# Kernel optimization log

Hardware: AMD Instinct MI355X
Metric: run time of the kernel (lower is better)

The kernel has to match this reference:

```python
import jax, jax.numpy as jnp
import numpy as np

B = 1024        # batch_size (len(c_ids))
D = 128         # dim_proto
N_AFE_A = 2     # len(AFE_a_ids_selected) == l_a
N_AFE_R = 2     # len(AFE_r_ids_selected) == l_r
S = 16          # sum(n_nbs_per_hop) = 10 + 6
A = 4096        # num_atoms (active codebook rows)
L = N_AFE_A + N_AFE_R * S  # 34


def _normalize(x, eps=1e-12):
    # torch F.normalize(dim=-1): x / max(||x||_2, eps)
    n = jnp.linalg.norm(x, axis=-1, keepdims=True)
    return x / jnp.maximum(n, eps)


def setup_inputs() -> dict:
    key = jax.random.key(0)
    k1, k2, k3 = jax.random.split(key, 3)
    embeddings = jax.random.normal(k1, (B, L, D), dtype=jnp.float32)
    atoms = jax.random.uniform(k2, (A, D), dtype=jnp.float32, minval=0.0, maxval=0.5)
    W_att = jax.random.normal(k3, ((N_AFE_A + N_AFE_R * S) * D, N_AFE_R * S + N_AFE_A), dtype=jnp.float32) * 0.02
    b_att = jnp.zeros((N_AFE_R * S + N_AFE_A,), dtype=jnp.float32)
    return {"embeddings": embeddings, "atoms": atoms, "W_att": W_att, "b_att": b_att}


def reference(embeddings, atoms, W_att, b_att):
    atoms_n = _normalize(atoms)  # F.normalize(self.atoms[0:num_atoms], dim=-1), [A, D]

    # --- attribute emb sets: embeddings[:, i, :] for i in range(n_AFE_a) ---
    attr = embeddings[:, :N_AFE_A, :]                                 # [B, la, D]
    soft_a = jnp.einsum('bld,ad->bla', attr, atoms_n)                 # similarity vs codebook
    hard_a = (soft_a == soft_a.max(axis=-1, keepdims=True)).astype(jnp.float32)
    assoc_a = jnp.einsum('bla,ad->bld', hard_a, atoms)                # one-hot @ atoms (lookup)

    # --- relational emb sets: chunks of size S, flattened to [B*S, D] in torch ---
    rel = embeddings[:, N_AFE_A:, :].reshape(B, N_AFE_R, S, D)
    soft_r = jnp.einsum('brsd,ad->brsa', rel, atoms_n)
    hard_r = (soft_r == soft_r.max(axis=-1, keepdims=True)).astype(jnp.float32)
    assoc_r = jnp.einsum('brsa,ad->brsd', hard_r, atoms).reshape(B, N_AFE_R * S, D)

    # per-row L2 normalize each associated prototype, then concat along slot dim
    assoc = jnp.concatenate([_normalize(assoc_a), _normalize(assoc_r)], axis=1)  # [B, la+lr*S, D]

    # attention aggregation: Linear over flattened slots, then bmm
    a = assoc.reshape(B, (N_AFE_A + N_AFE_R * S) * D)
    att = a @ W_att + b_att                                           # [B, la+lr*S]
    obj_embs = _normalize(jnp.einsum('bl,bld->bd', att, assoc))       # [B, D]
    return obj_embs
```

## Files before the change

kernel.cpp:

```cpp
#include <hip/hip_runtime.h>
#include <math.h>

#define BB 1024
#define LL 34
#define DD 128
#define AA 4096
#define NROWS (BB * LL)
#define RTILES (NROWS / 16)
#define ATILES (AA / 16)
#define NSPLIT 8
#define TPS (ATILES / NSPLIT)
#define NCHUNK (TPS / 4)
#define TAU 2.5e-3f
#define SCOREBLKS ((RTILES / 16) * NSPLIT)
#define GTABBLKS (LL * 32)

typedef _Float16 f16;
typedef _Float16 f16x8 __attribute__((ext_vector_type(8)));
typedef float f32x4  __attribute__((ext_vector_type(4)));

#define OFF_EMBA   0u
#define OFF_ATOMB  8912896u
#define OFF_WFRAG  9961472u
#define OFF_G      10379264u
#define OFF_PQ     30433280u
#define OFF_INVN64 34889728u
#define OFF_INVNF  34922496u

__global__ __launch_bounds__(256) void k_prep(const float* __restrict__ emb,
                                              const float* __restrict__ atoms,
                                              const float* __restrict__ W,
                                              double* __restrict__ invn64,
                                              float* __restrict__ invnF,
                                              f16x8* __restrict__ embA,
                                              f16x8* __restrict__ atomB,
                                              f16x8* __restrict__ wfrag) {
    __shared__ __align__(16) float stbuf[4608];
    __shared__ double part[16][17];
    const int bid = blockIdx.x;
    const int tid = threadIdx.x;

    if (bid < RTILES + ATILES) {
        const bool isAtom = (bid >= RTILES);
        const int tile = isAtom ? bid - RTILES : bid;
        const float* src = (isAtom ? atoms : emb) + (size_t)tile * 2048;
        float4* st4 = (float4*)stbuf;
        for (int i = tid; i < 512; i += 256) {
            int row = i >> 5, c4 = i & 31;
            st4[row * 33 + c4] = ((const float4*)src)[i];
        }
        __syncthreads();

        const int ks = tid >> 6, l = tid & 63;
        const int m = l & 15, koff4 = ((l >> 4) << 1) + (ks << 3);
        float4 f0 = st4[m * 33 + koff4];
        float4 f1 = st4[m * 33 + koff4 + 1];
        float xs[8] = {f0.x, f0.y, f0.z, f0.w, f1.x, f1.y, f1.z, f1.w};

        if (!isAtom) {
            f16x8 h;
            #pragma unroll
            for (int j = 0; j < 8; j++) h[j] = (f16)xs[j];
            embA[(size_t)(tile * 4 + ks) * 64 + l] = h;
        } else {
            double ssq = 0.0;
            #pragma unroll
            for (int j = 0; j < 8; j++) ssq += (double)xs[j] * xs[j];
            part[m][ks * 4 + (l >> 4)] = ssq;
            __syncthreads();
            double tot = 0.0;
            #pragma unroll
            for (int q = 0; q < 16; q++) tot += part[m][q];
            double n = sqrt(tot);
            if (n < 1e-12) n = 1e-12;
            double inv = 1.0 / n;
            float invf = (float)inv;
            f16x8 h;
            #pragma unroll
            for (int j = 0; j < 8; j++) h[j] = (f16)(xs[j] * invf);
            if (ks == 0 && (l >> 4) == 0) {
                invn64[tile * 16 + m] = inv;
                invnF[tile * 16 + m] = invf;
            }
            atomB[(size_t)(tile * 4 + ks) * 64 + l] = h;
        }
    } else {
        const int l = bid - RTILES - ATILES;
        const float* wsrc = W + (size_t)l * 128 * LL;
        for (int i = tid; i < 128 * LL; i += 256) {
            int row = i / LL, j = i - row * LL;
            stbuf[row * 35 + j] = wsrc[i];
        }
        __syncthreads();
        for (int s = tid; s < 768; s += 256) {
            int lane = s & 63, ksnt = s >> 6;
            int ks = ksnt & 3, nt = ksnt >> 2;
            int j = nt * 16 + (lane & 15);
            int kb = ks * 32 + ((lane >> 4) << 3);
            f16x8 h;
            if (j < LL) {
                #pragma unroll
                for (int jj = 0; jj < 8; jj++) h[jj] = (f16)stbuf[(kb + jj) * 35 + j];
            } else {
                #pragma unroll
                for (int jj = 0; jj < 8; jj++) h[jj] = (f16)0.f;
            }
            wfrag[(size_t)((l * 3 + nt) * 4 + ks) * 64 + lane] = h;
        }
    }
}

__global__ __launch_bounds__(256, 3) void k_score(const f16x8* __restrict__ embA,
                                                  const char* __restrict__ atomB,
                                                  const f16x8* __restrict__ wfrag,
                                                  float* __restrict__ G,
                                                  float4* __restrict__ pq) {
    __shared__ __align__(16) char shmem[32768];
    const int tid = threadIdx.x;
    const int w = tid >> 6, l = tid & 63;

    if (blockIdx.x >= SCOREBLKS) {
        const int gb = blockIdx.x - SCOREBLKS;
        const int ll = gb >> 5, ab = gb & 31;
        float* gs = (float*)shmem;

        f16x8 bw[3][4];
        #pragma unroll
        for (int nt = 0; nt < 3; nt++)
            #pragma unroll
            for (int ks = 0; ks < 4; ks++)
                bw[nt][ks] = wfrag[(size_t)((ll * 3 + nt) * 4 + ks) * 64 + l];

        const int col = l & 15, rq = (l >> 4) * 4;
        #pragma unroll
        for (int t = 0; t < 2; t++) {
            int atile = ab * 8 + w * 2 + t;
            f16x8 ah[4];
            #pragma unroll
            for (int ks = 0; ks < 4; ks++)
                ah[ks] = *(const f16x8*)(atomB + ((size_t)(atile * 4 + ks) * 64 + l) * 16);
            f32x4 acc[3];
            #pragma unroll
            for (int nt = 0; nt < 3; nt++) acc[nt] = (f32x4){0.f, 0.f, 0.f, 0.f};
            #pragma unroll
            for (int ks = 0; ks < 4; ks++)
                #pragma unroll
                for (int nt = 0; nt < 3; nt++)
                    acc[nt] = __builtin_amdgcn_mfma_f32_16x16x32_f16(ah[ks], bw[nt][ks], acc[nt], 0, 0, 0);
            int aloc0 = (w * 2 + t) * 16 + rq;
            #pragma unroll
            for (int nt = 0; nt < 3; nt++) {
                int j = nt * 16 + col;
                if (j < LL) {
                    #pragma unroll
                    for (int r = 0; r < 4; r++)
                        gs[(aloc0 + r) * 36 + j] = acc[nt][r];
                }
            }
        }
        __syncthreads();
        float* Gl = G + ((size_t)ll * 4096 + ab * 128) * 36;
        for (int i = tid; i < 128 * 36; i += 256) Gl[i] = gs[i];
        return;
    }

    char (*sbuf)[16384] = (char(*)[16384])shmem;
    const int sp = blockIdx.x / 136, rb = blockIdx.x - sp * 136;
    const int rt0 = rb * 16 + w * 4;

    f16x8 a[4][4];
    #pragma unroll
    for (int f = 0; f < 4; f++)
        #pragma unroll
        for (int ks = 0; ks < 4; ks++)
            a[f][ks] = embA[(size_t)((rt0 + f) * 4 + ks) * 64 + l];

    float v1[16], v2[16];
    #pragma unroll
    for (int s = 0; s < 16; s++) { v1[s] = -3e38f; v2[s] = -3e38f; }

    #define STAGE(C, BUF)                                                          \
        {                                                                          \
            size_t _tb = (size_t)(sp * TPS + (C) * 4) * 4096;                      \
            _Pragma("unroll")                                                      \
            for (int r = 0; r < 4; r++) {                                          \
                const char* _src = atomB + _tb + r * 4096;                         \
                uint32_t* _dst = (uint32_t*)(&sbuf[BUF][0] + r * 4096 + w * 1024); \
                __builtin_amdgcn_global_load_lds((const uint32_t*)(_src + tid * 16), \
                                                 _dst, 16, 0, 0);                  \
            }                                                                      \
        }

    STAGE(0, 0);
    __syncthreads();

    for (int c = 0; c < NCHUNK; c++) {
        const int buf = c & 1;
        if (c + 1 < NCHUNK) STAGE(c + 1, buf ^ 1);

        #pragma unroll
        for (int tt = 0; tt < 4; tt++) {
            f16x8 bh[4];
            #pragma unroll
            for (int ks = 0; ks < 4; ks++)
                bh[ks] = *(const f16x8*)(&sbuf[buf][0] + tt * 4096 + ks * 1024 + l * 16);
            f32x4 acc[4];
            #pragma unroll
            for (int f = 0; f < 4; f++) acc[f] = (f32x4){0.f, 0.f, 0.f, 0.f};
            #pragma unroll
            for (int ks = 0; ks < 4; ks++)
                #pragma unroll
                for (int f = 0; f < 4; f++)
                    acc[f] = __builtin_amdgcn_mfma_f32_16x16x32_f16(a[f][ks], bh[ks], acc[f], 0, 0, 0);
            const unsigned tl = (unsigned)(c * 4 + tt);
            #pragma unroll
            for (int f = 0; f < 4; f++)
                #pragma unroll
                for (int r = 0; r < 4; r++) {
                    int s = f * 4 + r;
                    float xq = __uint_as_float((__float_as_uint(acc[f][r]) & 0xFFFFFFE0u) | tl);
                    v2[s] = __builtin_amdgcn_fmed3f(xq, v1[s], v2[s]);
                    v1[s] = fmaxf(v1[s], xq);
                }
        }
        __syncthreads();
    }
    #undef STAGE

    float vv1[16], vv2[16];
    int jj1[16], jj2[16];
    const int col = l & 15;
    #pragma unroll
    for (int s = 0; s < 16; s++) {
        unsigned u1 = __float_as_uint(v1[s]);
        unsigned u2 = __float_as_uint(v2[s]);
        vv1[s] = __uint_as_float(u1 & 0xFFFFFFE0u);
        vv2[s] = __uint_as_float(u2 & 0xFFFFFFE0u);
        jj1[s] = (sp * TPS + (int)(u1 & 31u)) * 16 + col;
        jj2[s] = (sp * TPS + (int)(u2 & 31u)) * 16 + col;
    }

    #pragma unroll
    for (int m = 1; m <= 8; m <<= 1) {
        #pragma unroll
        for (int s = 0; s < 16; s++) {
            float ov1 = __shfl_xor(vv1[s], m);
            float ov2 = __shfl_xor(vv2[s], m);
            int   oi1 = __shfl_xor(jj1[s], m);
            int   oi2 = __shfl_xor(jj2[s], m);
            bool sel = ov1 > vv1[s];
            float lv  = sel ? vv1[s] : ov1;
            int   li  = sel ? jj1[s] : oi1;
            float wv2 = sel ? ov2 : vv2[s];
            int   wi2 = sel ? oi2 : jj2[s];
            vv1[s] = sel ? ov1 : vv1[s];
            jj1[s] = sel ? oi1 : jj1[s];
            bool s2 = lv > wv2;
            vv2[s] = s2 ? lv : wv2;
            jj2[s] = s2 ? li : wi2;
        }
    }

    if ((l & 15) == 0) {
        int q = l >> 4;
        #pragma unroll
        for (int f = 0; f < 4; f++)
            #pragma unroll
            for (int r = 0; r < 4; r++) {
                int s = f * 4 + r;
                int row = (rt0 + f) * 16 + q * 4 + r;
                float4 o;
                o.x = vv1[s];
                o.y = vv2[s];
                o.z = __int_as_float(jj1[s]);
                o.w = __int_as_float(jj2[s]);
                pq[(size_t)row * NSPLIT + sp] = o;
            }
    }
}

__global__ __launch_bounds__(256) void k_epilogue(const float4* __restrict__ pq,
                                                  const float* __restrict__ emb,
                                                  const float* __restrict__ atoms,
                                                  const double* __restrict__ invn64,
                                                  const float* __restrict__ invnF,
                                                  const float* __restrict__ G,
                                                  const float* __restrict__ b_att,
                                                  float* __restrict__ out) {
    __shared__ __align__(16) float assoc[LL * DD];
    __shared__ __align__(16) float4 pqS[LL][NSPLIT];
    __shared__ int   amaxS[LL];
    __shared__ float invS[LL];
    __shared__ float attS[LL];
    __shared__ float wsum[4][40];
    __shared__ float sqw[4];
    __shared__ int   flagCnt;
    __shared__ int   flagRow[LL];

    const int b = blockIdx.x, tid = threadIdx.x;
    const int wid = tid >> 6, lane = tid & 63;

    if (tid == 0) flagCnt = 0;
    for (int i = tid; i < LL * NSPLIT; i += 256)
        pqS[i >> 3][i & 7] = pq[(size_t)(b * LL + (i >> 3)) * NSPLIT + (i & 7)];
    __syncthreads();

    if (tid < LL) {
        float V1 = -3e38f, V2 = -3e38f;
        int I1 = 0;
        #pragma unroll
        for (int sp = 0; sp < NSPLIT; sp++) {
            float4 qv = pqS[tid][sp];
            float a1 = qv.x, a2 = qv.y;
            int   j1 = __float_as_int(qv.z);
            bool sel = a1 > V1;
            float lv  = sel ? V1 : a1;
            float wv2 = sel ? a2 : V2;
            V1 = sel ? a1 : V1;
            I1 = sel ? j1 : I1;
            V2 = fmaxf(lv, wv2);
        }
        amaxS[tid] = I1;
        if (V1 - V2 < TAU) {
            int k = atomicAdd(&flagCnt, 1);
            flagRow[k] = tid;
        }
    }
    __syncthreads();

    const int cnt = flagCnt;
    for (int fi = wid; fi < cnt; fi += 4) {
        int row = flagRow[fi];
        const float2 ev = ((const float2*)(emb + (size_t)(b * LL + row) * DD))[lane];
        double bestS = -1e300;
        int bestI = 0x7fffffff;
        for (int sp = 0; sp < NSPLIT; sp++) {
            float4 qv = pqS[row][sp];
            #pragma unroll
            for (int h = 0; h < 2; h++) {
                int idx = __float_as_int(h ? qv.w : qv.z);
                const float2 av = ((const float2*)(atoms + (size_t)idx * DD))[lane];
                double p = (double)ev.x * av.x + (double)ev.y * av.y;
                #pragma unroll
                for (int m = 1; m <= 32; m <<= 1) p += __shfl_xor(p, m);
                double sc = p * invn64[idx];
                if (sc > bestS || (sc == bestS && idx < bestI)) { bestS = sc; bestI = idx; }
            }
        }
        if (lane == 0) amaxS[row] = bestI;
    }
    __syncthreads();

    if (tid < LL) invS[tid] = invnF[amaxS[tid]];
    if (lane < LL) {
        float ga = 0.f;
        for (int ll = wid; ll < LL; ll += 4)
            ga += G[((size_t)ll * 4096 + amaxS[ll]) * 36 + lane];
        wsum[wid][lane] = ga;
    }
    __syncthreads();

    for (int idx = tid; idx < LL * DD; idx += 256) {
        int ll = idx >> 7, d = idx & 127;
        assoc[idx] = atoms[(size_t)amaxS[ll] * DD + d] * invS[ll];
    }
    if (tid < LL)
        attS[tid] = b_att[tid] + wsum[0][tid] + wsum[1][tid] + wsum[2][tid] + wsum[3][tid];
    __syncthreads();

    float o = 0.0f;
    if (tid < DD) {
        #pragma unroll
        for (int ll = 0; ll < LL; ll++) o = fmaf(attS[ll], assoc[ll * DD + tid], o);
    }
    float sq = (tid < DD) ? o * o : 0.0f;
    #pragma unroll
    for (int off = 32; off; off >>= 1) sq += __shfl_xor(sq, off);
    if (lane == 0) sqw[wid] = sq;
    __syncthreads();
    float tot = sqw[0] + sqw[1] + sqw[2] + sqw[3];
    float n = sqrtf(tot);
    float inv = 1.0f / fmaxf(n, 1e-12f);
    if (tid < DD) out[(size_t)b * DD + tid] = o * inv;
}

extern "C" void kernel_launch(void* const* d_in, const int* in_sizes, int n_in,
                              void* d_out, int out_size, void* d_ws, size_t ws_size,
                              hipStream_t stream) {
    const float* emb   = (const float*)d_in[0];
    const float* atoms = (const float*)d_in[1];
    const float* W     = (const float*)d_in[2];
    const float* b_att = (const float*)d_in[3];
    float* out = (float*)d_out;

    char* ws = (char*)d_ws;
    f16x8*  embA   = (f16x8*)(ws + OFF_EMBA);
    char*   atomB  = (char*)(ws + OFF_ATOMB);
    f16x8*  wfrag  = (f16x8*)(ws + OFF_WFRAG);
    float*  G      = (float*)(ws + OFF_G);
    float4* pq     = (float4*)(ws + OFF_PQ);
    double* invn64 = (double*)(ws + OFF_INVN64);
    float*  invnF  = (float*)(ws + OFF_INVNF);

    k_prep<<<RTILES + ATILES + LL, 256, 0, stream>>>(emb, atoms, W, invn64, invnF,
                                                     embA, (f16x8*)atomB, wfrag);
    k_score<<<SCOREBLKS + GTABBLKS, 256, 0, stream>>>(embA, atomB, wfrag, G, pq);
    k_epilogue<<<BB, 256, 0, stream>>>(pq, emb, atoms, invn64, invnF, G, b_att, out);
}
```

Before: 157.6 us.

## Load atom tiles directly into registers instead of staging through LDS

The score loop stops staging atom tiles into double-buffered shared memory with global_load_lds and per-chunk barriers. Each wave now loads its B fragments straight from global memory into registers, using a two-register software pipeline across tiles. This removes the LDS traffic and the __syncthreads calls. In exchange every wave fetches the same atom data on its own, which leans on L1/L2, and it uses more registers.

```diff
diff --git a/kernel.cpp b/kernel.cpp
--- a/kernel.cpp
+++ b/kernel.cpp
@@ -10,7 +10,6 @@
 #define ATILES (AA / 16)
 #define NSPLIT 8
 #define TPS (ATILES / NSPLIT)
-#define NCHUNK (TPS / 4)
 #define TAU 2.5e-3f
 #define SCOREBLKS ((RTILES / 16) * NSPLIT)
 #define GTABBLKS (LL * 32)
@@ -115,14 +114,13 @@
                                                   const f16x8* __restrict__ wfrag,
                                                   float* __restrict__ G,
                                                   float4* __restrict__ pq) {
-    __shared__ __align__(16) char shmem[32768];
     const int tid = threadIdx.x;
     const int w = tid >> 6, l = tid & 63;
 
     if (blockIdx.x >= SCOREBLKS) {
+        __shared__ __align__(16) float gs[128 * 36];
         const int gb = blockIdx.x - SCOREBLKS;
         const int ll = gb >> 5, ab = gb & 31;
-        float* gs = (float*)shmem;
 
         f16x8 bw[3][4];
         #pragma unroll
@@ -164,7 +162,6 @@
         return;
     }
 
-    char (*sbuf)[16384] = (char(*)[16384])shmem;
     const int sp = blockIdx.x / 136, rb = blockIdx.x - sp * 136;
     const int rt0 = rb * 16 + w * 4;
 
@@ -179,53 +176,47 @@
     #pragma unroll
     for (int s = 0; s < 16; s++) { v1[s] = -3e38f; v2[s] = -3e38f; }
 
-    #define STAGE(C, BUF)                                                          \
-        {                                                                          \
-            size_t _tb = (size_t)(sp * TPS + (C) * 4) * 4096;                      \
-            _Pragma("unroll")                                                      \
-            for (int r = 0; r < 4; r++) {                                          \
-                const char* _src = atomB + _tb + r * 4096;                         \
-                uint32_t* _dst = (uint32_t*)(&sbuf[BUF][0] + r * 4096 + w * 1024); \
-                __builtin_amdgcn_global_load_lds((const uint32_t*)(_src + tid * 16), \
-                                                 _dst, 16, 0, 0);                  \
-            }                                                                      \
-        }
-
-    STAGE(0, 0);
-    __syncthreads();
-
-    for (int c = 0; c < NCHUNK; c++) {
-        const int buf = c & 1;
-        if (c + 1 < NCHUNK) STAGE(c + 1, buf ^ 1);
-
-        #pragma unroll
-        for (int tt = 0; tt < 4; tt++) {
-            f16x8 bh[4];
-            #pragma unroll
-            for (int ks = 0; ks < 4; ks++)
-                bh[ks] = *(const f16x8*)(&sbuf[buf][0] + tt * 4096 + ks * 1024 + l * 16);
-            f32x4 acc[4];
-            #pragma unroll
-            for (int f = 0; f < 4; f++) acc[f] = (f32x4){0.f, 0.f, 0.f, 0.f};
-            #pragma unroll
-            for (int ks = 0; ks < 4; ks++)
-                #pragma unroll
-                for (int f = 0; f < 4; f++)
-                    acc[f] = __builtin_amdgcn_mfma_f32_16x16x32_f16(a[f][ks], bh[ks], acc[f], 0, 0, 0);
-            const unsigned tl = (unsigned)(c * 4 + tt);
-            #pragma unroll
-            for (int f = 0; f < 4; f++)
-                #pragma unroll
-                for (int r = 0; r < 4; r++) {
-                    int s = f * 4 + r;
-                    float xq = __uint_as_float((__float_as_uint(acc[f][r]) & 0xFFFFFFE0u) | tl);
-                    v2[s] = __builtin_amdgcn_fmed3f(xq, v1[s], v2[s]);
-                    v1[s] = fmaxf(v1[s], xq);
-                }
-        }
-        __syncthreads();
-    }
-    #undef STAGE
+    const f16x8* bbase = (const f16x8*)(atomB) + (size_t)sp * TPS * 256;
+
+    #define LOADT(BUF, T)                                            \
+        {                                                            \
+            _Pragma("unroll")                                        \
+            for (int ks = 0; ks < 4; ks++)                           \
+                BUF[ks] = bbase[(size_t)(T) * 256 + ks * 64 + l];    \
+        }
+
+    #define COMP(BUF, T)                                                          \
+        {                                                                         \
+            f32x4 acc[4];                                                         \
+            _Pragma("unroll")                                                     \
+            for (int f = 0; f < 4; f++) acc[f] = (f32x4){0.f, 0.f, 0.f, 0.f};     \
+            _Pragma("unroll")                                                     \
+            for (int ks = 0; ks < 4; ks++)                                        \
+                _Pragma("unroll")                                                 \
+                for (int f = 0; f < 4; f++)                                       \
+                    acc[f] = __builtin_amdgcn_mfma_f32_16x16x32_f16(a[f][ks], BUF[ks], acc[f], 0, 0, 0); \
+            const unsigned tl = (unsigned)(T);                                    \
+            _Pragma("unroll")                                                     \
+            for (int f = 0; f < 4; f++)                                           \
+                _Pragma("unroll")                                                 \
+                for (int r = 0; r < 4; r++) {                                     \
+                    int s = f * 4 + r;                                            \
+                    float xq = __uint_as_float((__float_as_uint(acc[f][r]) & 0xFFFFFFE0u) | tl); \
+                    v2[s] = __builtin_amdgcn_fmed3f(xq, v1[s], v2[s]);            \
+                    v1[s] = fmaxf(v1[s], xq);                                     \
+                }                                                                 \
+        }
+
+    f16x8 c0[4], c1[4];
+    LOADT(c0, 0);
+    for (int t = 0; t < TPS; t += 2) {
+        LOADT(c1, t + 1);
+        COMP(c0, t);
+        if (t + 2 < TPS) LOADT(c0, t + 2);
+        COMP(c1, t + 1);
+    }
+    #undef LOADT
+    #undef COMP
 
     float vv1[16], vv2[16];
     int jj1[16], jj2[16];
```

After: 153.5 us. 2.6% less time.
